# Performance work log

Hardware: AMD Instinct MI355X
Metric: run time of the kernel (lower is better)

The kernel has to match this reference:

```python
import jax, jax.numpy as jnp
import numpy as np

HIDDEN = 32
N_STEPS = 64  # fixed-step RK4 replaces adaptive Dopri5 (same MLP-eval structure)
STD = 0.1     # init_params: Linear weights ~ N(0, 0.1), biases = 0


def _mlp(w1, b1, w2, b2, w3, b3, y):
    # NODE.forward: fc1 -> relu -> fc2 -> relu -> fc3 (t is unused in the source)
    h = jax.nn.relu(y @ w1 + b1)
    h = jax.nn.relu(h @ w2 + b2)
    return h @ w3 + b3


def setup_inputs() -> dict:
    key = jax.random.key(0)
    ks = jax.random.split(key, 8)
    B, D = 131072, 3
    x = jax.random.normal(ks[0], (B, D), dtype=jnp.float32)
    # eval times in (0.1, 1.0], sorted like a posterior-sample schedule
    samples = jnp.sort(
        jax.random.uniform(ks[1], (8, 1), jnp.float32, 0.1, 1.0), axis=0)
    w1 = (STD * jax.random.normal(ks[2], (D, HIDDEN))).astype(jnp.float32)
    b1 = jnp.zeros((HIDDEN,), jnp.float32)
    w2 = (STD * jax.random.normal(ks[3], (HIDDEN, HIDDEN))).astype(jnp.float32)
    b2 = jnp.zeros((HIDDEN,), jnp.float32)
    w3 = (STD * jax.random.normal(ks[4], (HIDDEN, D))).astype(jnp.float32)
    b3 = jnp.zeros((D,), jnp.float32)
    w_out = (STD * jax.random.normal(ks[5], (D, 1))).astype(jnp.float32)
    b_out = jnp.zeros((1,), jnp.float32)
    return {"x": x, "samples": samples, "w1": w1, "b1": b1, "w2": w2,
            "b2": b2, "w3": w3, "b3": b3, "w_out": w_out, "b_out": b_out}


def reference(x, samples, w1, b1, w2, b2, w3, b3, w_out, b_out):
    t_eval = samples[:, 0]                     # (S,)
    max_T = jnp.max(t_eval)
    dt = max_T / N_STEPS

    def step(y, _):
        k1 = _mlp(w1, b1, w2, b2, w3, b3, y)
        k2 = _mlp(w1, b1, w2, b2, w3, b3, y + 0.5 * dt * k1)
        k3 = _mlp(w1, b1, w2, b2, w3, b3, y + 0.5 * dt * k2)
        k4 = _mlp(w1, b1, w2, b2, w3, b3, y + dt * k3)
        y_new = y + (dt / 6.0) * (k1 + 2.0 * k2 + 2.0 * k3 + k4)
        return y_new, y_new

    # traj[i] is the state at time (i+1)*dt; shape (N_STEPS, B, 3)
    _, traj = jax.lax.scan(jax.checkpoint(step), x, jnp.arange(N_STEPS))

    # gather states at the grid step nearest each eval time
    idx = jnp.clip(jnp.round(t_eval / dt).astype(jnp.int32) - 1, 0, N_STEPS - 1)
    y_eval = traj[idx]                         # (S, B, 3)

    # fc_layers readout -> act_vec (S, B, 1)
    return y_eval @ w_out + b_out
```

## Files before the change

kernel.cpp:

```cpp
#include <hip/hip_runtime.h>

#define NSTEPS 64

typedef __attribute__((ext_vector_type(4)))  float  float4_;
typedef __attribute__((ext_vector_type(2)))  __fp16 half2_;
typedef __attribute__((ext_vector_type(8)))  __fp16 half8_;

__device__ __forceinline__ half2_ relu_pk_f16(float a, float b) {
    half2_ h = __builtin_amdgcn_cvt_pkrtz(a, b);
    return __builtin_elementwise_max(h, (half2_)(__fp16)0);
}

__global__ __launch_bounds__(256, 6)
void ode_rk4_mfma(const float* __restrict__ x,
                  const float* __restrict__ samples,
                  const float* __restrict__ w1, const float* __restrict__ b1,
                  const float* __restrict__ w2, const float* __restrict__ b2,
                  const float* __restrict__ w3, const float* __restrict__ b3,
                  const float* __restrict__ w_out, const float* __restrict__ b_out,
                  float* __restrict__ out, int B)
{
    const int lane  = threadIdx.x & 63;
    const int w     = threadIdx.x >> 6;
    const int col16 = lane & 15;
    const int quad  = lane >> 4;

    const int rowBase = (blockIdx.x * 4 + w) * 16;
    const int row = rowBase + col16;

    auto sig = [](int p) -> int {
        int q = (p & 15) >> 2, r = p & 3;
        return q * 8 + r + ((p < 16) ? 0 : 4);
    };

    const float maxT = samples[7];
    const float dt   = maxT / 64.0f;
    const float dt2  = 0.5f * dt;
    const float dt6  = dt / 6.0f;

    union F { half2_ h2[4]; half8_ h8; };
    F A1h[2], A1f[2];
#pragma unroll
    for (int H = 0; H < 2; ++H) {
        if (quad == 0) {
            int u = sig(16 * H + col16);
            float v0 = w1[0 * 32 + u], v1 = w1[1 * 32 + u], v2 = w1[2 * 32 + u];
            float bb = b1[u];
            A1h[H].h2[0] = (half2_){(__fp16)v0, (__fp16)v1};
            A1h[H].h2[1] = (half2_){(__fp16)v2, (__fp16)bb};
            A1h[H].h2[2] = (half2_){(__fp16)(dt2 * v0), (__fp16)(dt2 * v1)};
            A1h[H].h2[3] = (half2_){(__fp16)(dt2 * v2), (__fp16)0.0f};
            A1f[H].h2[0] = A1h[H].h2[0];
            A1f[H].h2[1] = A1h[H].h2[1];
            A1f[H].h2[2] = (half2_){(__fp16)(dt * v0), (__fp16)(dt * v1)};
            A1f[H].h2[3] = (half2_){(__fp16)(dt * v2), (__fp16)0.0f};
        } else {
#pragma unroll
            for (int pp = 0; pp < 4; ++pp) {
                A1h[H].h2[pp] = (half2_)(__fp16)0.0f;
                A1f[H].h2[pp] = (half2_)(__fp16)0.0f;
            }
        }
    }

    F A2[2];
    float4_ Cb[2];
#pragma unroll
    for (int H = 0; H < 2; ++H) {
        int u = sig(16 * H + col16);
#pragma unroll
        for (int pp = 0; pp < 4; ++pp) {
            int kk = quad * 8 + 2 * pp;
            A2[H].h2[pp] = (half2_){(__fp16)w2[kk * 32 + u], (__fp16)w2[(kk + 1) * 32 + u]};
        }
#pragma unroll
        for (int r = 0; r < 4; ++r)
            Cb[H][r] = b2[sig(16 * H + quad * 4 + r)];
    }

    F A3;
    {
        const int  d    = col16 & 3;
        const bool live = d < 3;
#pragma unroll
        for (int pp = 0; pp < 4; ++pp) {
            int kk = quad * 8 + 2 * pp;
            A3.h2[pp] = live
                ? (half2_){(__fp16)w3[kk * 3 + d], (__fp16)w3[(kk + 1) * 3 + d]}
                : (half2_)(__fp16)0.0f;
        }
    }
    float4_ C3;
#pragma unroll
    for (int r = 0; r < 4; ++r)
        C3[r] = (r < 3) ? b3[r] : 0.0f;

    float4_ Zc;
#pragma unroll
    for (int r = 0; r < 4; ++r) Zc[r] = 0.0f;

    int sidx[8];
    unsigned long long smask = 0ull;
#pragma unroll
    for (int j = 0; j < 8; ++j) {
        int id = (int)rintf(samples[j] / dt) - 1;
        id = id < 0 ? 0 : (id > NSTEPS - 1 ? NSTEPS - 1 : id);
        id = __builtin_amdgcn_readfirstlane(id);
        sidx[j] = id;
        smask |= 1ull << id;
    }
    const float wo0 = w_out[0], wo1 = w_out[1], wo2 = w_out[2];
    const float bo  = b_out[0];

    float y0 = x[(size_t)row * 3 + 0];
    float y1 = x[(size_t)row * 3 + 1];
    float y2 = x[(size_t)row * 3 + 2];

    const half2_ zh = (half2_)(__fp16)0.0f;

#pragma unroll 1
    for (int s = 0; s < NSTEPS; ++s) {
        float acc0 = 0.f, acc1 = 0.f, acc2 = 0.f;

        half2_ yp01 = __builtin_amdgcn_cvt_pkrtz(y0, y1);
        half2_ yp2o = __builtin_amdgcn_cvt_pkrtz(y2, 1.0f);

        float k0 = 0.f, k1 = 0.f, k2 = 0.f;

#pragma unroll
        for (int st = 0; st < 4; ++st) {
            half2_ kp01 = (st == 0) ? zh : __builtin_amdgcn_cvt_pkrtz(k0, k1);
            half2_ kp2o = (st == 0) ? zh : __builtin_amdgcn_cvt_pkrtz(k2, 0.0f);
            F BL1;
            BL1.h2[0] = yp01; BL1.h2[1] = yp2o;
            BL1.h2[2] = kp01; BL1.h2[3] = kp2o;

            float4_ D1_0, D1_1;
            if (st == 3) {
                D1_0 = __builtin_amdgcn_mfma_f32_16x16x32_f16(A1f[0].h8, BL1.h8, Zc, 0, 0, 0);
                D1_1 = __builtin_amdgcn_mfma_f32_16x16x32_f16(A1f[1].h8, BL1.h8, Zc, 0, 0, 0);
            } else {
                D1_0 = __builtin_amdgcn_mfma_f32_16x16x32_f16(A1h[0].h8, BL1.h8, Zc, 0, 0, 0);
                D1_1 = __builtin_amdgcn_mfma_f32_16x16x32_f16(A1h[1].h8, BL1.h8, Zc, 0, 0, 0);
            }

            F P;
            P.h2[0] = relu_pk_f16(D1_0[0], D1_0[1]);
            P.h2[1] = relu_pk_f16(D1_0[2], D1_0[3]);
            P.h2[2] = relu_pk_f16(D1_1[0], D1_1[1]);
            P.h2[3] = relu_pk_f16(D1_1[2], D1_1[3]);

            float4_ D2_0 = __builtin_amdgcn_mfma_f32_16x16x32_f16(A2[0].h8, P.h8, Cb[0], 0, 0, 0);
            float4_ D2_1 = __builtin_amdgcn_mfma_f32_16x16x32_f16(A2[1].h8, P.h8, Cb[1], 0, 0, 0);

            F Q;
            Q.h2[0] = relu_pk_f16(D2_0[0], D2_0[1]);
            Q.h2[1] = relu_pk_f16(D2_0[2], D2_0[3]);
            Q.h2[2] = relu_pk_f16(D2_1[0], D2_1[1]);
            Q.h2[3] = relu_pk_f16(D2_1[2], D2_1[3]);

            float4_ D3 = __builtin_amdgcn_mfma_f32_16x16x32_f16(A3.h8, Q.h8, C3, 0, 0, 0);

            k0 = D3[0];
            k1 = D3[1];
            k2 = D3[2];

            const float ca = (st == 1 || st == 2) ? 2.0f : 1.0f;
            acc0 = fmaf(ca, k0, acc0); acc1 = fmaf(ca, k1, acc1); acc2 = fmaf(ca, k2, acc2);
        }
        y0 = fmaf(dt6, acc0, y0); y1 = fmaf(dt6, acc1, y1); y2 = fmaf(dt6, acc2, y2);

        if ((smask >> s) & 1ull) {
            if (quad == 0) {
#pragma unroll
                for (int j = 0; j < 8; ++j) {
                    if (sidx[j] == s) {
                        out[(size_t)j * B + row] = fmaf(y2, wo2, fmaf(y1, wo1, fmaf(y0, wo0, bo)));
                    }
                }
            }
        }
    }
}

extern "C" void kernel_launch(void* const* d_in, const int* in_sizes, int n_in,
                              void* d_out, int out_size, void* d_ws, size_t ws_size,
                              hipStream_t stream) {
    const float* x       = (const float*)d_in[0];
    const float* samples = (const float*)d_in[1];
    const float* w1      = (const float*)d_in[2];
    const float* b1      = (const float*)d_in[3];
    const float* w2      = (const float*)d_in[4];
    const float* b2      = (const float*)d_in[5];
    const float* w3      = (const float*)d_in[6];
    const float* b3      = (const float*)d_in[7];
    const float* w_out   = (const float*)d_in[8];
    const float* b_out   = (const float*)d_in[9];
    float* out = (float*)d_out;

    const int B = in_sizes[0] / 3;
    const int rowsPerBlock = 64;
    const int grid = (B + rowsPerBlock - 1) / rowsPerBlock;
    ode_rk4_mfma<<<grid, 256, 0, stream>>>(
        x, samples, w1, b1, w2, b2, w3, b3, w_out, b_out, out, B);
}
```

Before: 215.2 us.

## Fold fc3 into next-stage fc1 and sum RK4 stages before fc3

Precomputes W3·W1 scaled by dt/2 and dt so each later RK stage's first-layer input comes from the previous hidden activations. The y-only first-layer products for all stages are issued up front, where they do not depend on one another. The fc3 output layer is applied once per step to an fp16 weighted sum of the hidden states instead of once per stage. This shortens the serial MFMA dependency chain and drops three fc3 MFMAs per step, but accumulates the stage sum in fp16, which may cost accuracy. Launch bounds occupancy hint lowered from 6 to 4.

```diff
diff --git a/kernel.cpp b/kernel.cpp
--- a/kernel.cpp
+++ b/kernel.cpp
@@ -11,7 +11,7 @@
     return __builtin_elementwise_max(h, (half2_)(__fp16)0);
 }
 
-__global__ __launch_bounds__(256, 6)
+__global__ __launch_bounds__(256, 4)
 void ode_rk4_mfma(const float* __restrict__ x,
                   const float* __restrict__ samples,
                   const float* __restrict__ w1, const float* __restrict__ b1,
@@ -39,27 +39,37 @@
     const float dt6  = dt / 6.0f;
 
     union F { half2_ h2[4]; half8_ h8; };
-    F A1h[2], A1f[2];
+
+    F A1y[2];
 #pragma unroll
     for (int H = 0; H < 2; ++H) {
         if (quad == 0) {
             int u = sig(16 * H + col16);
-            float v0 = w1[0 * 32 + u], v1 = w1[1 * 32 + u], v2 = w1[2 * 32 + u];
-            float bb = b1[u];
-            A1h[H].h2[0] = (half2_){(__fp16)v0, (__fp16)v1};
-            A1h[H].h2[1] = (half2_){(__fp16)v2, (__fp16)bb};
-            A1h[H].h2[2] = (half2_){(__fp16)(dt2 * v0), (__fp16)(dt2 * v1)};
-            A1h[H].h2[3] = (half2_){(__fp16)(dt2 * v2), (__fp16)0.0f};
-            A1f[H].h2[0] = A1h[H].h2[0];
-            A1f[H].h2[1] = A1h[H].h2[1];
-            A1f[H].h2[2] = (half2_){(__fp16)(dt * v0), (__fp16)(dt * v1)};
-            A1f[H].h2[3] = (half2_){(__fp16)(dt * v2), (__fp16)0.0f};
+            A1y[H].h2[0] = (half2_){(__fp16)w1[0 * 32 + u], (__fp16)w1[1 * 32 + u]};
+            A1y[H].h2[1] = (half2_){(__fp16)w1[2 * 32 + u], (__fp16)b1[u]};
+            A1y[H].h2[2] = (half2_)(__fp16)0.0f;
+            A1y[H].h2[3] = (half2_)(__fp16)0.0f;
         } else {
 #pragma unroll
-            for (int pp = 0; pp < 4; ++pp) {
-                A1h[H].h2[pp] = (half2_)(__fp16)0.0f;
-                A1f[H].h2[pp] = (half2_)(__fp16)0.0f;
-            }
+            for (int pp = 0; pp < 4; ++pp) A1y[H].h2[pp] = (half2_)(__fp16)0.0f;
+        }
+    }
+
+    F Mh[2], Mf[2];
+#pragma unroll
+    for (int H = 0; H < 2; ++H) {
+        int u = sig(16 * H + col16);
+#pragma unroll
+        for (int pp = 0; pp < 4; ++pp) {
+            int kk = quad * 8 + 2 * pp;
+            float m0 = w3[kk * 3 + 0] * w1[0 * 32 + u]
+                     + w3[kk * 3 + 1] * w1[1 * 32 + u]
+                     + w3[kk * 3 + 2] * w1[2 * 32 + u];
+            float m1 = w3[(kk + 1) * 3 + 0] * w1[0 * 32 + u]
+                     + w3[(kk + 1) * 3 + 1] * w1[1 * 32 + u]
+                     + w3[(kk + 1) * 3 + 2] * w1[2 * 32 + u];
+            Mh[H].h2[pp] = (half2_){(__fp16)(dt2 * m0), (__fp16)(dt2 * m1)};
+            Mf[H].h2[pp] = (half2_){(__fp16)(dt  * m0), (__fp16)(dt  * m1)};
         }
     }
 
@@ -93,7 +103,7 @@
     float4_ C3;
 #pragma unroll
     for (int r = 0; r < 4; ++r)
-        C3[r] = (r < 3) ? b3[r] : 0.0f;
+        C3[r] = (r < 3) ? 6.0f * b3[r] : 0.0f;
 
     float4_ Zc;
 #pragma unroll
@@ -111,64 +121,82 @@
     }
     const float wo0 = w_out[0], wo1 = w_out[1], wo2 = w_out[2];
     const float bo  = b_out[0];
+    const float cH0 = dt2 * b3[0], cH1 = dt2 * b3[1], cH2 = dt2 * b3[2];
+    const float cF0 = dt  * b3[0], cF1 = dt  * b3[1], cF2 = dt  * b3[2];
 
     float y0 = x[(size_t)row * 3 + 0];
     float y1 = x[(size_t)row * 3 + 1];
     float y2 = x[(size_t)row * 3 + 2];
 
-    const half2_ zh = (half2_)(__fp16)0.0f;
-
 #pragma unroll 1
     for (int s = 0; s < NSTEPS; ++s) {
-        float acc0 = 0.f, acc1 = 0.f, acc2 = 0.f;
-
-        half2_ yp01 = __builtin_amdgcn_cvt_pkrtz(y0, y1);
-        half2_ yp2o = __builtin_amdgcn_cvt_pkrtz(y2, 1.0f);
-
-        float k0 = 0.f, k1 = 0.f, k2 = 0.f;
-
-#pragma unroll
-        for (int st = 0; st < 4; ++st) {
-            half2_ kp01 = (st == 0) ? zh : __builtin_amdgcn_cvt_pkrtz(k0, k1);
-            half2_ kp2o = (st == 0) ? zh : __builtin_amdgcn_cvt_pkrtz(k2, 0.0f);
-            F BL1;
-            BL1.h2[0] = yp01; BL1.h2[1] = yp2o;
-            BL1.h2[2] = kp01; BL1.h2[3] = kp2o;
-
+        half2_ b0a = __builtin_amdgcn_cvt_pkrtz(y0, y1);
+        half2_ b0b = __builtin_amdgcn_cvt_pkrtz(y2, 1.0f);
+        half2_ bHa = __builtin_amdgcn_cvt_pkrtz(y0 + cH0, y1 + cH1);
+        half2_ bHb = __builtin_amdgcn_cvt_pkrtz(y2 + cH2, 1.0f);
+        half2_ bFa = __builtin_amdgcn_cvt_pkrtz(y0 + cF0, y1 + cF1);
+        half2_ bFb = __builtin_amdgcn_cvt_pkrtz(y2 + cF2, 1.0f);
+        F By0, ByH, ByF;
+        By0.h2[0] = b0a; By0.h2[1] = b0b; By0.h2[2] = b0a; By0.h2[3] = b0b;
+        ByH.h2[0] = bHa; ByH.h2[1] = bHb; ByH.h2[2] = bHa; ByH.h2[3] = bHb;
+        ByF.h2[0] = bFa; ByF.h2[1] = bFb; ByF.h2[2] = bFa; ByF.h2[3] = bFb;
+
+        float4_ D1s0_0 = __builtin_amdgcn_mfma_f32_16x16x32_f16(A1y[0].h8, By0.h8, Zc, 0, 0, 0);
+        float4_ D1s0_1 = __builtin_amdgcn_mfma_f32_16x16x32_f16(A1y[1].h8, By0.h8, Zc, 0, 0, 0);
+        float4_ DbH0   = __builtin_amdgcn_mfma_f32_16x16x32_f16(A1y[0].h8, ByH.h8, Zc, 0, 0, 0);
+        float4_ DbH1   = __builtin_amdgcn_mfma_f32_16x16x32_f16(A1y[1].h8, ByH.h8, Zc, 0, 0, 0);
+        float4_ DbF0   = __builtin_amdgcn_mfma_f32_16x16x32_f16(A1y[0].h8, ByF.h8, Zc, 0, 0, 0);
+        float4_ DbF1   = __builtin_amdgcn_mfma_f32_16x16x32_f16(A1y[1].h8, ByF.h8, Zc, 0, 0, 0);
+
+        F Q, Sacc;
+
+        {
+            F P;
+            P.h2[0] = relu_pk_f16(D1s0_0[0], D1s0_0[1]);
+            P.h2[1] = relu_pk_f16(D1s0_0[2], D1s0_0[3]);
+            P.h2[2] = relu_pk_f16(D1s0_1[0], D1s0_1[1]);
+            P.h2[3] = relu_pk_f16(D1s0_1[2], D1s0_1[3]);
+            float4_ D2_0 = __builtin_amdgcn_mfma_f32_16x16x32_f16(A2[0].h8, P.h8, Cb[0], 0, 0, 0);
+            float4_ D2_1 = __builtin_amdgcn_mfma_f32_16x16x32_f16(A2[1].h8, P.h8, Cb[1], 0, 0, 0);
+            Q.h2[0] = relu_pk_f16(D2_0[0], D2_0[1]);
+            Q.h2[1] = relu_pk_f16(D2_0[2], D2_0[3]);
+            Q.h2[2] = relu_pk_f16(D2_1[0], D2_1[1]);
+            Q.h2[3] = relu_pk_f16(D2_1[2], D2_1[3]);
+#pragma unroll
+            for (int pp = 0; pp < 4; ++pp) Sacc.h2[pp] = Q.h2[pp];
+        }
+
+#pragma unroll
+        for (int st = 1; st < 4; ++st) {
             float4_ D1_0, D1_1;
             if (st == 3) {
-                D1_0 = __builtin_amdgcn_mfma_f32_16x16x32_f16(A1f[0].h8, BL1.h8, Zc, 0, 0, 0);
-                D1_1 = __builtin_amdgcn_mfma_f32_16x16x32_f16(A1f[1].h8, BL1.h8, Zc, 0, 0, 0);
+                D1_0 = __builtin_amdgcn_mfma_f32_16x16x32_f16(Mf[0].h8, Q.h8, DbF0, 0, 0, 0);
+                D1_1 = __builtin_amdgcn_mfma_f32_16x16x32_f16(Mf[1].h8, Q.h8, DbF1, 0, 0, 0);
             } else {
-                D1_0 = __builtin_amdgcn_mfma_f32_16x16x32_f16(A1h[0].h8, BL1.h8, Zc, 0, 0, 0);
-                D1_1 = __builtin_amdgcn_mfma_f32_16x16x32_f16(A1h[1].h8, BL1.h8, Zc, 0, 0, 0);
+                D1_0 = __builtin_amdgcn_mfma_f32_16x16x32_f16(Mh[0].h8, Q.h8, DbH0, 0, 0, 0);
+                D1_1 = __builtin_amdgcn_mfma_f32_16x16x32_f16(Mh[1].h8, Q.h8, DbH1, 0, 0, 0);
             }
-
             F P;
             P.h2[0] = relu_pk_f16(D1_0[0], D1_0[1]);
             P.h2[1] = relu_pk_f16(D1_0[2], D1_0[3]);
             P.h2[2] = relu_pk_f16(D1_1[0], D1_1[1]);
             P.h2[3] = relu_pk_f16(D1_1[2], D1_1[3]);
-
             float4_ D2_0 = __builtin_amdgcn_mfma_f32_16x16x32_f16(A2[0].h8, P.h8, Cb[0], 0, 0, 0);
             float4_ D2_1 = __builtin_amdgcn_mfma_f32_16x16x32_f16(A2[1].h8, P.h8, Cb[1], 0, 0, 0);
-
-            F Q;
             Q.h2[0] = relu_pk_f16(D2_0[0], D2_0[1]);
             Q.h2[1] = relu_pk_f16(D2_0[2], D2_0[3]);
             Q.h2[2] = relu_pk_f16(D2_1[0], D2_1[1]);
             Q.h2[3] = relu_pk_f16(D2_1[2], D2_1[3]);
-
-            float4_ D3 = __builtin_amdgcn_mfma_f32_16x16x32_f16(A3.h8, Q.h8, C3, 0, 0, 0);
-
-            k0 = D3[0];
-            k1 = D3[1];
-            k2 = D3[2];
-
-            const float ca = (st == 1 || st == 2) ? 2.0f : 1.0f;
-            acc0 = fmaf(ca, k0, acc0); acc1 = fmaf(ca, k1, acc1); acc2 = fmaf(ca, k2, acc2);
-        }
-        y0 = fmaf(dt6, acc0, y0); y1 = fmaf(dt6, acc1, y1); y2 = fmaf(dt6, acc2, y2);
+            const __fp16 ca = (st == 3) ? (__fp16)1.0f : (__fp16)2.0f;
+#pragma unroll
+            for (int pp = 0; pp < 4; ++pp)
+                Sacc.h2[pp] += ca * Q.h2[pp];
+        }
+
+        float4_ D3 = __builtin_amdgcn_mfma_f32_16x16x32_f16(A3.h8, Sacc.h8, C3, 0, 0, 0);
+        y0 = fmaf(dt6, D3[0], y0);
+        y1 = fmaf(dt6, D3[1], y1);
+        y2 = fmaf(dt6, D3[2], y2);
 
         if ((smask >> s) & 1ull) {
             if (quad == 0) {
```

Result: no change. 211.3 us (-1.8%).
